# Optimization experiments

Hardware: AMD Instinct MI355X
Metric: run time of the kernel (lower is better)

Reference implementation:

```python
import jax, jax.numpy as jnp
import numpy as np

Q = 8
T, N, M = 16, 128, 128
K = 5
C_IN = 2 + T            # x, y, and T solution timesteps stacked as channels
C_HID = 2 * (4 + Q)     # 24
C_OUT = 4 + Q           # kappa, v1, v2, f, q RK-stage fields
DT = 1.0


def _conv(h, W, b):
    # h: (C, N, M), W: (O, C, K, K) -> (O, N, M), SAME padding (padding = K//2)
    o = jax.lax.conv_general_dilated(h[None], W, (1, 1), 'SAME',
                                     dimension_numbers=('NCHW', 'OIHW', 'NCHW'))[0]
    return o + b[:, None, None]


def setup_inputs() -> dict:
    key = jax.random.key(0)
    ks = jax.random.split(key, 12)
    def w(k, o, c):
        return jax.random.normal(k, (o, c, K, K), jnp.float32) * (1.0 / np.sqrt(c * K * K))
    return {
        'x': jax.random.normal(ks[0], (N, M), jnp.float32),
        'y': jax.random.normal(ks[1], (N, M), jnp.float32),
        'u': jax.random.normal(ks[2], (T, N, M), jnp.float32),
        'W1': w(ks[3], C_HID, C_IN), 'b1': jnp.zeros((C_HID,), jnp.float32),
        'W2': w(ks[4], C_HID, C_HID), 'b2': jnp.zeros((C_HID,), jnp.float32),
        'W3': w(ks[5], C_HID, C_HID), 'b3': jnp.zeros((C_HID,), jnp.float32),
        'W4': w(ks[6], C_HID, C_HID), 'b4': jnp.zeros((C_HID,), jnp.float32),
        'W5': w(ks[7], C_OUT, C_HID), 'b5': jnp.zeros((C_OUT,), jnp.float32),
        'rk_A': jax.random.normal(ks[8], (Q, Q), jnp.float32) * 0.05,
        'rk_b': jax.random.normal(ks[9], (Q,), jnp.float32) * 0.05,
    }


def reference(x, y, u, W1, b1, W2, b2, W3, b3, W4, b4, W5, b5, rk_A, rk_b):
    def net(xx, yy):
        h = jnp.concatenate([xx[None], yy[None], u], axis=0)  # (2+T, N, M)
        h = jax.nn.relu(_conv(h, W1, b1))
        h = jax.nn.relu(_conv(h, W2, b2))
        h = jax.nn.relu(_conv(h, W3, b3))
        h = jax.nn.relu(_conv(h, W4, b4))
        return _conv(h, W5, b5)  # (C_OUT, N, M)

    outs, vjp = jax.vjp(net, x, y)
    kappa, v1, v2, f = outs[0], outs[1], outs[2], outs[3]
    u_rk = outs[4:]  # (Q, N, M)

    # one-hot channel cotangents for kappa, v1, v2 and the Q RK-stage fields
    idx = jnp.array([0, 1, 2] + list(range(4, 4 + Q)))
    n_cot = idx.shape[0]
    cots = jnp.zeros((n_cot, C_OUT, N, M), outs.dtype).at[jnp.arange(n_cot), idx].set(1.0)

    # batched first-order VJPs (replaces the torch autograd.grad loop)
    gx, gy = jax.vmap(vjp)(cots)
    kappa_x, v1_x, v2_x = gx[0], gx[1], gx[2]
    kappa_y, v1_y, v2_y = gy[0], gy[1], gy[2]
    u_rk_x, u_rk_y = gx[3:], gy[3:]  # (Q, N, M)

    ones = jnp.ones((N, M), outs.dtype)
    cot_u = cots[3:]

    def du_x(xx, c):
        return jax.vjp(lambda a: net(a, y), xx)[1](c)[0]

    def du_y(yy, c):
        return jax.vjp(lambda a: net(x, a), yy)[1](c)[0]

    # second derivatives: VJP of the first-derivative map, batched over RK stages
    u_rk_xx = jax.vmap(lambda c: jax.vjp(lambda a: du_x(a, c), x)[1](ones)[0])(cot_u)
    u_rk_yy = jax.vmap(lambda c: jax.vjp(lambda a: du_y(a, c), y)[1](ones)[0])(cot_u)

    pde = (kappa[None] * (u_rk_xx + u_rk_yy)
           + kappa_x[None] * u_rk_x + kappa_y[None] * u_rk_y
           + v1[None] * u_rk_x + v2[None] * u_rk_y
           + f[None])

    uhat_i = u_rk + DT * jnp.einsum('ij,jkl->ikl', rk_A, pde)
    uhat_f = u_rk + DT * jnp.einsum('ij,jkl->ikl', rk_A - rk_b[None, :], pde)

    # all outputs of the torch forward, stacked along channel dim: (2Q+10, N, M)
    return jnp.concatenate([
        uhat_i, uhat_f,
        kappa[None], kappa_x[None], kappa_y[None],
        v1[None], v1_x[None], v1_y[None],
        v2[None], v2_x[None], v2_y[None],
        f[None]], axis=0)
```

## Files before the change

### kernel.cpp

```cpp
#include <hip/hip_runtime.h>

static constexpr int P = 16384;

static constexpr int OFF_H1   = 0;
static constexpr int OFF_H2   = 24 * P;
static constexpr int OFF_H3   = 48 * P;
static constexpr int OFF_H4   = 72 * P;
static constexpr int OFF_OUT5 = 96 * P;
static constexpr int OFF_GA   = 108 * P;
static constexpr int OFF_GB   = 372 * P;
static constexpr int OFF_DXY  = 636 * P;
static constexpr int OFF_W    = 658 * P;

static constexpr int PW1 = 0;
static constexpr int PW2 = 10800;
static constexpr int PW3 = 25200;
static constexpr int PW4 = 39600;
static constexpr int PW5 = 54000;
static constexpr int PB4 = 61200;
static constexpr int PB3 = 75600;
static constexpr int PB2 = 90000;
static constexpr int PB1 = 104400;

__global__ void pack_weights(const float* __restrict__ W1, const float* __restrict__ W2,
                             const float* __restrict__ W3, const float* __restrict__ W4,
                             const float* __restrict__ W5, float* __restrict__ wp) {
    int i = blockIdx.x * 256 + threadIdx.x;
    if (i < 10800) {
        int co = i % 24, ci = (i / 24) % 18, t = i / 432;
        wp[PW1 + i] = W1[(co * 18 + ci) * 25 + t];
    }
    if (i < 14400) {
        int co = i % 24, ci = (i / 24) % 24, t = i / 576;
        wp[PW2 + i] = W2[(co * 24 + ci) * 25 + t];
        wp[PW3 + i] = W3[(co * 24 + ci) * 25 + t];
        wp[PW4 + i] = W4[(co * 24 + ci) * 25 + t];
        int cin = i % 24, cout = (i / 24) % 24, tb = i / 576;
        wp[PB4 + i] = W4[(cout * 24 + cin) * 25 + (24 - tb)];
        wp[PB3 + i] = W3[(cout * 24 + cin) * 25 + (24 - tb)];
        wp[PB2 + i] = W2[(cout * 24 + cin) * 25 + (24 - tb)];
    }
    if (i < 7200) {
        int co = i % 12, ci = (i / 12) % 24, t = i / 288;
        wp[PW5 + i] = W5[(co * 24 + ci) * 25 + t];
    }
    if (i < 1200) {
        int ci = i % 2, co = (i / 2) % 24, t = i / 48;
        wp[PB1 + i] = W1[(co * 18 + ci) * 25 + (24 - t)];
    }
}

__global__ void stage_input(const float* __restrict__ x, const float* __restrict__ y,
                            const float* __restrict__ u, float* __restrict__ in18) {
    int i = blockIdx.x * 256 + threadIdx.x;
    int pl = i / P, p = i - pl * P;
    float v = (pl == 0) ? x[p] : (pl == 1) ? y[p] : u[(pl - 2) * P + p];
    in18[i] = v;
}

template <int CIN, int CHUNK, int COUT_TOT, int COB, bool RELU, bool MASK, bool BATCH>
__global__ __launch_bounds__(256, 7) void conv5x5(
    const float* __restrict__ inbase, const float* __restrict__ wp,
    const float* __restrict__ bias, const float* __restrict__ maskbase,
    float* __restrict__ outbase) {
    constexpr int NSPL = COUT_TOT / COB;
    const int z = blockIdx.z;
    const int half = z % NSPL;
    const int cot = z / NSPL;
    const float* in = inbase + (BATCH ? cot * CIN * P : 0);
    float* out = outbase + (BATCH ? cot * COUT_TOT * P : 0);
    const int cobase = half * COB;

    __shared__ float smem[CHUNK][20][24];
    const int tid = threadIdx.x;
    const int bx = blockIdx.x, by = blockIdx.y;
    const int ty = tid >> 4, tx = tid & 15;

    float acc[COB];
#pragma unroll
    for (int co = 0; co < COB; ++co) acc[co] = bias ? bias[cobase + co] : 0.f;

    for (int c0 = 0; c0 < CIN; c0 += CHUNK) {
        if (c0) __syncthreads();
        for (int i = tid; i < CHUNK * 400; i += 256) {
            int ci = i / 400, rem = i - ci * 400;
            int r = rem / 20, c = rem - r * 20;
            int gy = by * 16 + r - 2, gx = bx * 16 + c - 2;
            float v = 0.f;
            if ((unsigned)gy < 128u && (unsigned)gx < 128u)
                v = in[(c0 + ci) * P + gy * 128 + gx];
            smem[ci][r][c] = v;
        }
        __syncthreads();

        for (int a = 0; a < 5; ++a) {
            for (int b = 0; b < 5; ++b) {
                const float* __restrict__ wrow =
                    wp + ((a * 5 + b) * CIN + c0) * COUT_TOT + cobase;
                for (int ci = 0; ci < CHUNK; ++ci) {
                    float v = smem[ci][ty + a][tx + b];
#pragma unroll
                    for (int co = 0; co < COB; ++co)
                        acc[co] = fmaf(v, wrow[ci * COUT_TOT + co], acc[co]);
                }
            }
        }
    }

    const int gy = by * 16 + ty, gx = bx * 16 + tx, gp = gy * 128 + gx;
#pragma unroll
    for (int co = 0; co < COB; ++co) {
        float v = acc[co];
        if (RELU) v = v > 0.f ? v : 0.f;
        if (MASK) v = (maskbase[(cobase + co) * P + gp] > 0.f) ? v : 0.f;
        out[(cobase + co) * P + gp] = v;
    }
}

__global__ __launch_bounds__(256) void bcot_init(const float* __restrict__ W5,
                                                 const float* __restrict__ h4,
                                                 float* __restrict__ gA) {
    const int i = blockIdx.z;
    const int oc = (i < 3) ? i : i + 1;
    const int tid = threadIdx.x;
    const int gy = blockIdx.y * 16 + (tid >> 4);
    const int gx = blockIdx.x * 16 + (tid & 15);
    const int gp = gy * 128 + gx;
    float* g = gA + i * 24 * P;
    for (int j = 0; j < 24; ++j) {
        const float* __restrict__ w = W5 + (oc * 24 + j) * 25;
        float s = 0.f;
        for (int a = 0; a < 5; ++a) {
            int yy = gy + 2 - a;
            if ((unsigned)yy >= 128u) continue;
            for (int b = 0; b < 5; ++b) {
                int xx = gx + 2 - b;
                if ((unsigned)xx >= 128u) continue;
                s += w[a * 5 + b];
            }
        }
        g[j * P + gp] = (h4[j * P + gp] > 0.f) ? s : 0.f;
    }
}

__global__ __launch_bounds__(256) void finalize(const float* __restrict__ ws,
                                                const float* __restrict__ rkA,
                                                const float* __restrict__ rkb,
                                                float* __restrict__ outp) {
    const int p = blockIdx.x * 256 + threadIdx.x;
    const float* o5 = ws + OFF_OUT5;
    const float* dxy = ws + OFF_DXY;

    const float kap = o5[0 * P + p], v1 = o5[1 * P + p];
    const float v2  = o5[2 * P + p], f  = o5[3 * P + p];
    const float kx  = dxy[0 * P + p], ky  = dxy[1 * P + p];
    const float v1x = dxy[2 * P + p], v1y = dxy[3 * P + p];
    const float v2x = dxy[4 * P + p], v2y = dxy[5 * P + p];
    const float cx = kx + v1, cy = ky + v2;

    float pde[8], urk[8];
#pragma unroll
    for (int q = 0; q < 8; ++q) {
        urk[q] = o5[(4 + q) * P + p];
        float ux = dxy[(6 + 2 * q) * P + p];
        float uy = dxy[(7 + 2 * q) * P + p];
        pde[q] = fmaf(cx, ux, fmaf(cy, uy, f));
    }
#pragma unroll
    for (int r = 0; r < 8; ++r) {
        float si = 0.f, sf = 0.f;
#pragma unroll
        for (int j = 0; j < 8; ++j) {
            float a = rkA[r * 8 + j];
            si = fmaf(a, pde[j], si);
            sf = fmaf(a - rkb[j], pde[j], sf);
        }
        outp[r * P + p] = urk[r] + si;
        outp[(8 + r) * P + p] = urk[r] + sf;
    }
    outp[16 * P + p] = kap;
    outp[17 * P + p] = kx;
    outp[18 * P + p] = ky;
    outp[19 * P + p] = v1;
    outp[20 * P + p] = v1x;
    outp[21 * P + p] = v1y;
    outp[22 * P + p] = v2;
    outp[23 * P + p] = v2x;
    outp[24 * P + p] = v2y;
    outp[25 * P + p] = f;
}

extern "C" void kernel_launch(void* const* d_in, const int* in_sizes, int n_in,
                              void* d_out, int out_size, void* d_ws, size_t ws_size,
                              hipStream_t stream) {
    const float* x   = (const float*)d_in[0];
    const float* y   = (const float*)d_in[1];
    const float* u   = (const float*)d_in[2];
    const float* W1  = (const float*)d_in[3];
    const float* b1  = (const float*)d_in[4];
    const float* W2  = (const float*)d_in[5];
    const float* b2  = (const float*)d_in[6];
    const float* W3  = (const float*)d_in[7];
    const float* b3  = (const float*)d_in[8];
    const float* W4  = (const float*)d_in[9];
    const float* b4  = (const float*)d_in[10];
    const float* W5  = (const float*)d_in[11];
    const float* b5  = (const float*)d_in[12];
    const float* rkA = (const float*)d_in[13];
    const float* rkb = (const float*)d_in[14];

    float* ws   = (float*)d_ws;
    float* outp = (float*)d_out;
    float* wp   = ws + OFF_W;

    pack_weights<<<dim3(57), dim3(256), 0, stream>>>(W1, W2, W3, W4, W5, wp);
    stage_input<<<dim3(18 * 64), dim3(256), 0, stream>>>(x, y, u, ws + OFF_GB);

    dim3 blk(256);
    conv5x5<18, 9, 24, 4, true, false, false><<<dim3(8, 8, 6), blk, 0, stream>>>(
        ws + OFF_GB, wp + PW1, b1, nullptr, ws + OFF_H1);
    conv5x5<24, 12, 24, 4, true, false, false><<<dim3(8, 8, 6), blk, 0, stream>>>(
        ws + OFF_H1, wp + PW2, b2, nullptr, ws + OFF_H2);
    conv5x5<24, 12, 24, 4, true, false, false><<<dim3(8, 8, 6), blk, 0, stream>>>(
        ws + OFF_H2, wp + PW3, b3, nullptr, ws + OFF_H3);
    conv5x5<24, 12, 24, 4, true, false, false><<<dim3(8, 8, 6), blk, 0, stream>>>(
        ws + OFF_H3, wp + PW4, b4, nullptr, ws + OFF_H4);
    conv5x5<24, 12, 12, 4, false, false, false><<<dim3(8, 8, 3), blk, 0, stream>>>(
        ws + OFF_H4, wp + PW5, b5, nullptr, ws + OFF_OUT5);

    bcot_init<<<dim3(8, 8, 11), blk, 0, stream>>>(W5, ws + OFF_H4, ws + OFF_GA);
    conv5x5<24, 12, 24, 12, false, true, true><<<dim3(8, 8, 22), blk, 0, stream>>>(
        ws + OFF_GA, wp + PB4, nullptr, ws + OFF_H3, ws + OFF_GB);
    conv5x5<24, 12, 24, 12, false, true, true><<<dim3(8, 8, 22), blk, 0, stream>>>(
        ws + OFF_GB, wp + PB3, nullptr, ws + OFF_H2, ws + OFF_GA);
    conv5x5<24, 12, 24, 12, false, true, true><<<dim3(8, 8, 22), blk, 0, stream>>>(
        ws + OFF_GA, wp + PB2, nullptr, ws + OFF_H1, ws + OFF_GB);
    conv5x5<24, 12, 2, 2, false, false, true><<<dim3(8, 8, 11), blk, 0, stream>>>(
        ws + OFF_GB, wp + PB1, nullptr, nullptr, ws + OFF_DXY);

    finalize<<<dim3(64), blk, 0, stream>>>(ws, rkA, rkb, outp);
}
```

Baseline: 600.3 us.

## Fuse backward cotangent init into first backward conv and shrink backward tiles

The separate bcot_init kernel is removed. A small table of border-clipped W5 window sums is precomputed in pack_weights, and the first backward conv builds its input on the fly from that table, masked by the h4 activation. The backward convs also move to 8-row tiles with 128 threads, doubling the block count for better occupancy and load balance. The shared tile drops its padding columns, going from 24 to 20, which may raise bank conflicts.

```diff
diff --git a/kernel.cpp b/kernel.cpp
--- a/kernel.cpp
+++ b/kernel.cpp
@@ -24,7 +24,8 @@
 
 __global__ void pack_weights(const float* __restrict__ W1, const float* __restrict__ W2,
                              const float* __restrict__ W3, const float* __restrict__ W4,
-                             const float* __restrict__ W5, float* __restrict__ wp) {
+                             const float* __restrict__ W5, float* __restrict__ wp,
+                             float* __restrict__ tbl) {
     int i = blockIdx.x * 256 + threadIdx.x;
     if (i < 10800) {
         int co = i % 24, ci = (i / 24) % 18, t = i / 432;
@@ -48,6 +49,17 @@
         int ci = i % 2, co = (i / 2) % 24, t = i / 48;
         wp[PB1 + i] = W1[(co * 18 + ci) * 25 + (24 - t)];
     }
+    if (i < 6600) {
+        int cx = i % 5, cy = (i / 5) % 5, ci = (i / 25) % 24, cot = i / 600;
+        int oc = (cot < 3) ? cot : cot + 1;
+        int a0 = (cy <= 2) ? 0 : cy - 2, a1 = (cy >= 2) ? 4 : cy + 2;
+        int b0 = (cx <= 2) ? 0 : cx - 2, b1 = (cx >= 2) ? 4 : cx + 2;
+        const float* __restrict__ w = W5 + (oc * 24 + ci) * 25;
+        float s = 0.f;
+        for (int a = a0; a <= a1; ++a)
+            for (int b = b0; b <= b1; ++b) s += w[a * 5 + b];
+        tbl[i] = s;
+    }
 }
 
 __global__ void stage_input(const float* __restrict__ x, const float* __restrict__ y,
@@ -58,20 +70,23 @@
     in18[i] = v;
 }
 
-template <int CIN, int CHUNK, int COUT_TOT, int COB, bool RELU, bool MASK, bool BATCH>
-__global__ __launch_bounds__(256, 7) void conv5x5(
+template <int TH, int CIN, int CHUNK, int COUT_TOT, int COB,
+          bool RELU, bool MASK, bool BATCH, bool TBL>
+__global__ __launch_bounds__(TH * 16, 7) void conv5x5(
     const float* __restrict__ inbase, const float* __restrict__ wp,
     const float* __restrict__ bias, const float* __restrict__ maskbase,
-    float* __restrict__ outbase) {
+    const float* __restrict__ tbl, float* __restrict__ outbase) {
     constexpr int NSPL = COUT_TOT / COB;
+    constexpr int HR = TH + 4;
+    constexpr int NT = TH * 16;
     const int z = blockIdx.z;
     const int half = z % NSPL;
     const int cot = z / NSPL;
-    const float* in = inbase + (BATCH ? cot * CIN * P : 0);
+    const float* in = inbase + ((BATCH && !TBL) ? cot * CIN * P : 0);
     float* out = outbase + (BATCH ? cot * COUT_TOT * P : 0);
     const int cobase = half * COB;
 
-    __shared__ float smem[CHUNK][20][24];
+    __shared__ float smem[CHUNK][HR][20];
     const int tid = threadIdx.x;
     const int bx = blockIdx.x, by = blockIdx.y;
     const int ty = tid >> 4, tx = tid & 15;
@@ -82,13 +97,23 @@
 
     for (int c0 = 0; c0 < CIN; c0 += CHUNK) {
         if (c0) __syncthreads();
-        for (int i = tid; i < CHUNK * 400; i += 256) {
-            int ci = i / 400, rem = i - ci * 400;
+        for (int i = tid; i < CHUNK * HR * 20; i += NT) {
+            int ci = i / (HR * 20), rem = i - ci * (HR * 20);
             int r = rem / 20, c = rem - r * 20;
-            int gy = by * 16 + r - 2, gx = bx * 16 + c - 2;
+            int gy = by * TH + r - 2, gx = bx * 16 + c - 2;
             float v = 0.f;
-            if ((unsigned)gy < 128u && (unsigned)gx < 128u)
-                v = in[(c0 + ci) * P + gy * 128 + gx];
+            if ((unsigned)gy < 128u && (unsigned)gx < 128u) {
+                if (TBL) {
+                    float m = in[(c0 + ci) * P + gy * 128 + gx];
+                    if (m > 0.f) {
+                        int cy = (gy < 2) ? gy : (gy > 125) ? gy - 123 : 2;
+                        int cx = (gx < 2) ? gx : (gx > 125) ? gx - 123 : 2;
+                        v = tbl[((cot * CIN + c0 + ci) * 5 + cy) * 5 + cx];
+                    }
+                } else {
+                    v = in[(c0 + ci) * P + gy * 128 + gx];
+                }
+            }
             smem[ci][r][c] = v;
         }
         __syncthreads();
@@ -107,39 +132,13 @@
         }
     }
 
-    const int gy = by * 16 + ty, gx = bx * 16 + tx, gp = gy * 128 + gx;
+    const int gy = by * TH + ty, gx = bx * 16 + tx, gp = gy * 128 + gx;
 #pragma unroll
     for (int co = 0; co < COB; ++co) {
         float v = acc[co];
         if (RELU) v = v > 0.f ? v : 0.f;
         if (MASK) v = (maskbase[(cobase + co) * P + gp] > 0.f) ? v : 0.f;
         out[(cobase + co) * P + gp] = v;
-    }
-}
-
-__global__ __launch_bounds__(256) void bcot_init(const float* __restrict__ W5,
-                                                 const float* __restrict__ h4,
-                                                 float* __restrict__ gA) {
-    const int i = blockIdx.z;
-    const int oc = (i < 3) ? i : i + 1;
-    const int tid = threadIdx.x;
-    const int gy = blockIdx.y * 16 + (tid >> 4);
-    const int gx = blockIdx.x * 16 + (tid & 15);
-    const int gp = gy * 128 + gx;
-    float* g = gA + i * 24 * P;
-    for (int j = 0; j < 24; ++j) {
-        const float* __restrict__ w = W5 + (oc * 24 + j) * 25;
-        float s = 0.f;
-        for (int a = 0; a < 5; ++a) {
-            int yy = gy + 2 - a;
-            if ((unsigned)yy >= 128u) continue;
-            for (int b = 0; b < 5; ++b) {
-                int xx = gx + 2 - b;
-                if ((unsigned)xx >= 128u) continue;
-                s += w[a * 5 + b];
-            }
-        }
-        g[j * P + gp] = (h4[j * P + gp] > 0.f) ? s : 0.f;
     }
 }
 
@@ -212,31 +211,31 @@
     float* ws   = (float*)d_ws;
     float* outp = (float*)d_out;
     float* wp   = ws + OFF_W;
-
-    pack_weights<<<dim3(57), dim3(256), 0, stream>>>(W1, W2, W3, W4, W5, wp);
+    float* tbl  = ws + OFF_GA;
+
+    pack_weights<<<dim3(57), dim3(256), 0, stream>>>(W1, W2, W3, W4, W5, wp, tbl);
     stage_input<<<dim3(18 * 64), dim3(256), 0, stream>>>(x, y, u, ws + OFF_GB);
 
-    dim3 blk(256);
-    conv5x5<18, 9, 24, 4, true, false, false><<<dim3(8, 8, 6), blk, 0, stream>>>(
-        ws + OFF_GB, wp + PW1, b1, nullptr, ws + OFF_H1);
-    conv5x5<24, 12, 24, 4, true, false, false><<<dim3(8, 8, 6), blk, 0, stream>>>(
-        ws + OFF_H1, wp + PW2, b2, nullptr, ws + OFF_H2);
-    conv5x5<24, 12, 24, 4, true, false, false><<<dim3(8, 8, 6), blk, 0, stream>>>(
-        ws + OFF_H2, wp + PW3, b3, nullptr, ws + OFF_H3);
-    conv5x5<24, 12, 24, 4, true, false, false><<<dim3(8, 8, 6), blk, 0, stream>>>(
-        ws + OFF_H3, wp + PW4, b4, nullptr, ws + OFF_H4);
-    conv5x5<24, 12, 12, 4, false, false, false><<<dim3(8, 8, 3), blk, 0, stream>>>(
-        ws + OFF_H4, wp + PW5, b5, nullptr, ws + OFF_OUT5);
-
-    bcot_init<<<dim3(8, 8, 11), blk, 0, stream>>>(W5, ws + OFF_H4, ws + OFF_GA);
-    conv5x5<24, 12, 24, 12, false, true, true><<<dim3(8, 8, 22), blk, 0, stream>>>(
-        ws + OFF_GA, wp + PB4, nullptr, ws + OFF_H3, ws + OFF_GB);
-    conv5x5<24, 12, 24, 12, false, true, true><<<dim3(8, 8, 22), blk, 0, stream>>>(
-        ws + OFF_GB, wp + PB3, nullptr, ws + OFF_H2, ws + OFF_GA);
-    conv5x5<24, 12, 24, 12, false, true, true><<<dim3(8, 8, 22), blk, 0, stream>>>(
-        ws + OFF_GA, wp + PB2, nullptr, ws + OFF_H1, ws + OFF_GB);
-    conv5x5<24, 12, 2, 2, false, false, true><<<dim3(8, 8, 11), blk, 0, stream>>>(
-        ws + OFF_GB, wp + PB1, nullptr, nullptr, ws + OFF_DXY);
-
-    finalize<<<dim3(64), blk, 0, stream>>>(ws, rkA, rkb, outp);
-}
+    dim3 blk256(256), blk128(128);
+    conv5x5<16, 18, 9, 24, 4, true, false, false, false><<<dim3(8, 8, 6), blk256, 0, stream>>>(
+        ws + OFF_GB, wp + PW1, b1, nullptr, nullptr, ws + OFF_H1);
+    conv5x5<16, 24, 12, 24, 4, true, false, false, false><<<dim3(8, 8, 6), blk256, 0, stream>>>(
+        ws + OFF_H1, wp + PW2, b2, nullptr, nullptr, ws + OFF_H2);
+    conv5x5<16, 24, 12, 24, 4, true, false, false, false><<<dim3(8, 8, 6), blk256, 0, stream>>>(
+        ws + OFF_H2, wp + PW3, b3, nullptr, nullptr, ws + OFF_H3);
+    conv5x5<16, 24, 12, 24, 4, true, false, false, false><<<dim3(8, 8, 6), blk256, 0, stream>>>(
+        ws + OFF_H3, wp + PW4, b4, nullptr, nullptr, ws + OFF_H4);
+    conv5x5<16, 24, 12, 12, 4, false, false, false, false><<<dim3(8, 8, 3), blk256, 0, stream>>>(
+        ws + OFF_H4, wp + PW5, b5, nullptr, nullptr, ws + OFF_OUT5);
+
+    conv5x5<8, 24, 12, 24, 12, false, true, true, true><<<dim3(8, 16, 22), blk128, 0, stream>>>(
+        ws + OFF_H4, wp + PB4, nullptr, ws + OFF_H3, tbl, ws + OFF_GB);
+    conv5x5<8, 24, 12, 24, 12, false, true, true, false><<<dim3(8, 16, 22), blk128, 0, stream>>>(
+        ws + OFF_GB, wp + PB3, nullptr, ws + OFF_H2, nullptr, ws + OFF_GA);
+    conv5x5<8, 24, 12, 24, 12, false, true, true, false><<<dim3(8, 16, 22), blk128, 0, stream>>>(
+        ws + OFF_GA, wp + PB2, nullptr, ws + OFF_H1, nullptr, ws + OFF_GB);
+    conv5x5<8, 24, 12, 2, 2, false, false, true, false><<<dim3(8, 16, 11), blk128, 0, stream>>>(
+        ws + OFF_GB, wp + PB1, nullptr, nullptr, nullptr, ws + OFF_DXY);
+
+    finalize<<<dim3(64), blk256, 0, stream>>>(ws, rkA, rkb, outp);
+}
```

New measurement: 584.8 us. -2.6%, faster.
